# Performance work log

Hardware: AMD Instinct MI355X
Metric: run time of the kernel (lower is better)

## Reference

```python
import jax, jax.numpy as jnp
import numpy as np

B, S, D, NH, NKV, HD = 1, 2048, 4096, 32, 8, 128
SCALE = HD ** -0.5


def setup_inputs() -> dict:
    key = jax.random.key(0)
    ks = jax.random.split(key, 5)
    sd = D ** -0.5
    x = jax.random.normal(ks[0], (B, S, D), jnp.float32)
    Wq = jax.random.normal(ks[1], (D, NH * HD), jnp.float32) * sd
    Wk = jax.random.normal(ks[2], (D, NKV * HD), jnp.float32) * sd
    Wv = jax.random.normal(ks[3], (D, NKV * HD), jnp.float32) * sd
    Wo = jax.random.normal(ks[4], (NH * HD, D), jnp.float32) * sd
    # real rotary tables (rotate-half convention), shape [S, HD]
    inv_freq = 1.0 / (10000.0 ** (np.arange(0, HD, 2, dtype=np.float64) / HD))
    ang = np.outer(np.arange(S, dtype=np.float64), inv_freq)  # [S, HD//2]
    emb = np.concatenate([ang, ang], axis=-1)  # [S, HD]
    cos = jnp.asarray(np.cos(emb), jnp.float32)
    sin = jnp.asarray(np.sin(emb), jnp.float32)
    return dict(x=x, Wq=Wq, Wk=Wk, Wv=Wv, Wo=Wo, cos=cos, sin=sin)


def _rope(t, cos, sin):
    # t: [B,S,H,HD]; cos/sin: [S,HD]
    c = cos[None, :, None, :]
    s = sin[None, :, None, :]
    t1, t2 = jnp.split(t, 2, axis=-1)
    rot = jnp.concatenate([-t2, t1], axis=-1)
    return t * c + rot * s


def _to_i8(t):
    # per-vector absmax quantization over last dim
    scale = 127.0 / jnp.clip(jnp.max(jnp.abs(t), axis=-1, keepdims=True), 1e-5, None)
    q = jnp.clip(jnp.round(t * scale), -128.0, 127.0).astype(jnp.int8)
    return q, scale


def reference(x, Wq, Wk, Wv, Wo, cos, sin):
    q = (x @ Wq).reshape(B, S, NH, HD)
    k = (x @ Wk).reshape(B, S, NKV, HD)
    v = (x @ Wv).reshape(B, S, NKV, HD)
    q = _rope(q, cos, sin)
    k = _rope(k, cos, sin)
    q_i8, q_s = _to_i8(q)          # [B,S,NH,HD], [B,S,NH,1]
    k_i8, k_s = _to_i8(k)          # [B,S,NKV,HD], [B,S,NKV,1]
    rep = NH // NKV                # GQA expansion
    k_i8 = jnp.repeat(k_i8, rep, axis=2)
    k_s = jnp.repeat(k_s, rep, axis=2)
    v = jnp.repeat(v, rep, axis=2)
    # int8 QK^T accumulated in int32 (exact), then per-vector dequant
    scores = jnp.einsum('bshd,bthd->bhst', q_i8, k_i8,
                        preferred_element_type=jnp.int32).astype(jnp.float32)
    q_st = jnp.transpose(q_s, (0, 2, 1, 3))            # [B,NH,S,1]
    k_st = jnp.transpose(k_s, (0, 2, 3, 1))            # [B,NH,1,S]
    scores = scores * (SCALE / (q_st * k_st))
    # causal mask (seq > 1, no cache so total == S)
    mask = jnp.triu(jnp.full((S, S), -jnp.inf, jnp.float32), k=1)
    scores = scores + mask
    attn = jax.nn.softmax(scores, axis=-1)             # [B,NH,S,S]
    out = jnp.einsum('bhst,bthd->bshd', attn, v).reshape(B, S, NH * HD)
    return out @ Wo
```

## Files before the change

### kernel.cpp

```cpp
#include <hip/hip_runtime.h>
#include <hip/hip_bf16.h>

#define S_LEN 2048
#define DMODEL 4096
#define NH 32
#define NKV 8
#define HD 128
#define NQKV 6144
#define VOFF (DMODEL + NKV * HD)
#define ATT_SCALE_L2E 0.1275175213528852f

typedef __bf16 bf16x8 __attribute__((ext_vector_type(8)));
typedef __bf16 bf16x4 __attribute__((ext_vector_type(4)));
typedef float f32x4 __attribute__((ext_vector_type(4)));
typedef int i32x4 __attribute__((ext_vector_type(4)));

template <bool B> struct BoolC { static constexpr bool value = B; };

__device__ __forceinline__ unsigned short f2b(float f) {
  union { float f; unsigned u; } a; a.f = f;
  unsigned u = a.u;
  return (unsigned short)((u + 0x7FFFu + ((u >> 16) & 1u)) >> 16);
}
__device__ __forceinline__ float b2f(unsigned short u) {
  union { unsigned u; float f; } a; a.u = (unsigned)u << 16; return a.f;
}

__device__ __forceinline__ void gl16(const void* g, void* l) {
  __builtin_amdgcn_global_load_lds(
      (const __attribute__((address_space(1))) unsigned int*)g,
      (__attribute__((address_space(3))) unsigned int*)l, 16, 0, 0);
}

__global__ __launch_bounds__(256) void k_prep(const float* __restrict__ x,
                                              const float* __restrict__ Wq,
                                              const float* __restrict__ Wk,
                                              const float* __restrict__ Wv,
                                              const float* __restrict__ Wo,
                                              unsigned short* __restrict__ xb,
                                              unsigned short* __restrict__ wqkv_t,
                                              unsigned short* __restrict__ wo_t) {
  __shared__ float tile[64][65];
  const int id = blockIdx.x;
  if (id >= 10240) {
    int i = (id - 10240) * 256 + threadIdx.x;
    float4 v = ((const float4*)x)[i];
    ushort4 o;
    o.x = f2b(v.x); o.y = f2b(v.y); o.z = f2b(v.z); o.w = f2b(v.w);
    ((ushort4*)xb)[i] = o;
    return;
  }
  const float* W;
  unsigned short* Wt;
  int N, bx, by;
  if (id < 4096)      { W = Wq; Wt = wqkv_t;                         N = 4096; bx = id & 63;          by = id >> 6; }
  else if (id < 5120) { W = Wk; Wt = wqkv_t + (size_t)4096 * 4096;   N = 1024; bx = (id - 4096) & 63; by = (id - 4096) >> 6; }
  else if (id < 6144) { W = Wv; Wt = wqkv_t + (size_t)5120 * 4096;   N = 1024; bx = (id - 5120) & 63; by = (id - 5120) >> 6; }
  else                { W = Wo; Wt = wo_t;                           N = 4096; bx = (id - 6144) & 63; by = (id - 6144) >> 6; }
  const int k0 = bx * 64, n0 = by * 64;
  const int tx = threadIdx.x & 31, ty = threadIdx.x >> 5;
#pragma unroll
  for (int i = 0; i < 8; ++i) {
    int k = ty + i * 8;
    const float* src = W + (size_t)(k0 + k) * N + n0;
    tile[k][tx] = src[tx];
    tile[k][tx + 32] = src[tx + 32];
  }
  __syncthreads();
  int kq = threadIdx.x & 15, nb = threadIdx.x >> 4;
#pragma unroll
  for (int i = 0; i < 4; ++i) {
    int n = nb + i * 16;
    ushort4 o;
    o.x = f2b(tile[kq * 4 + 0][n]);
    o.y = f2b(tile[kq * 4 + 1][n]);
    o.z = f2b(tile[kq * 4 + 2][n]);
    o.w = f2b(tile[kq * 4 + 3][n]);
    *(ushort4*)&Wt[(size_t)(n0 + n) * 4096 + k0 + kq * 4] = o;
  }
}

__global__ __launch_bounds__(256) void k_post(const unsigned short* __restrict__ qkv,
                                              const float* __restrict__ cost,
                                              const float* __restrict__ sint,
                                              signed char* __restrict__ q_i8,
                                              float* __restrict__ q_ds_t,
                                              signed char* __restrict__ k_i8,
                                              float* __restrict__ k_ds_t,
                                              unsigned short* __restrict__ v_t) {
  __shared__ unsigned short tile[64][65];
  const int id = blockIdx.x;
  if (id < 20480) {
    int y = id >> 11, s = id & 2047;
    int wv = threadIdx.x >> 6, l = threadIdx.x & 63;
    int hh = y * 4 + wv;
    const unsigned short* row = qkv + (size_t)s * NQKV;
    int off = (hh < NH) ? hh * HD : DMODEL + (hh - NH) * HD;
    float t1 = b2f(row[off + l]), t2 = b2f(row[off + 64 + l]);
    float c1 = cost[s * HD + l],      sn1 = sint[s * HD + l];
    float c2 = cost[s * HD + 64 + l], sn2 = sint[s * HD + 64 + l];
    float o1 = t1 * c1 - t2 * sn1;
    float o2 = t2 * c2 + t1 * sn2;
    float amax = fmaxf(fabsf(o1), fabsf(o2));
#pragma unroll
    for (int m = 1; m < 64; m <<= 1) amax = fmaxf(amax, __shfl_xor(amax, m));
    amax = fmaxf(amax, 1e-5f);
    float scale = 127.0f / amax;
    float dscale = amax * (1.0f / 127.0f);
    float v1 = fminf(fmaxf(rintf(o1 * scale), -128.f), 127.f);
    float v2 = fminf(fmaxf(rintf(o2 * scale), -128.f), 127.f);
    if (hh < NH) {
      signed char* dst = q_i8 + ((size_t)s * NH + hh) * HD;
      dst[l] = (signed char)v1; dst[l + 64] = (signed char)v2;
      if (l == 0) q_ds_t[(size_t)hh * S_LEN + s] = dscale;
    } else {
      int kh = hh - NH;
      signed char* dst = k_i8 + ((size_t)s * NKV + kh) * HD;
      dst[l] = (signed char)v1; dst[l + 64] = (signed char)v2;
      if (l == 0) k_ds_t[(size_t)kh * S_LEN + s] = dscale;
    }
    return;
  }
  int vid = id - 20480;
  int s0 = (vid & 31) * 64, d0 = ((vid >> 5) & 1) * 64, kvh = vid >> 6;
  int tx = threadIdx.x & 63, ty = threadIdx.x >> 6;
#pragma unroll
  for (int i = 0; i < 16; ++i) {
    int s = ty + i * 4;
    tile[s][tx] = qkv[(size_t)(s0 + s) * NQKV + VOFF + kvh * HD + d0 + tx];
  }
  __syncthreads();
#pragma unroll
  for (int i = 0; i < 16; ++i) {
    int d = ty + i * 4;
    v_t[((size_t)kvh * HD + d0 + d) * S_LEN + s0 + tx] = tile[tx][d];
  }
}

__global__ __launch_bounds__(512, 4) void k_g128x3(const unsigned short* __restrict__ A,
                                                   const unsigned short* __restrict__ B,
                                                   unsigned short* __restrict__ C,
                                                   int M, int N, int K) {
  constexpr int FN = 3;
  extern __shared__ __align__(16) unsigned short smem[];
  char* Sc = (char*)smem;
  const int tid = threadIdx.x;
  const int wvid = tid >> 6, l = tid & 63;
  const int wm = wvid >> 2, wn = wvid & 3;
  const int l15 = l & 15, l4 = l >> 4;

  const int cpx = gridDim.x >> 3;
  const int swz = (blockIdx.x & 7) * cpx + (blockIdx.x >> 3);
  const int mtiles = M >> 7;
  const int m0 = (swz % mtiles) * 128;
  const int n0 = (swz / mtiles) * (FN * 64);

  const int NT = K >> 6;

  const int rsw = (l15 & 7) << 4;
  const int a_base = (wm * 64 + l15) * 128;
  const int b_base = (wn * FN * 16 + l15) * 128;
  const int c0 = (l4 * 16) ^ rsw;
  const int c1 = (64 + l4 * 16) ^ rsw;

  const int srow = l >> 3;
  const int st_k8 = (l & 7) ^ (srow & 7);

  auto stA = [&](int tt) {
    if (tt >= NT) return;
    const unsigned short* g = A + (size_t)(m0 + wvid * 8 + srow) * K + tt * 64 + st_k8 * 8;
    char* lb = Sc + (tt & 1) * 16384 + wvid * 1024;
#pragma unroll
    for (int j = 0; j < 2; ++j)
      gl16(g + (size_t)(j * 64) * K, (unsigned short*)(lb + j * 8192));
  };
  auto stB = [&](int tt) {
    if (tt >= NT) return;
    const unsigned short* g = B + (size_t)(n0 + wvid * 8 + srow) * K + tt * 64 + st_k8 * 8;
    char* lb = Sc + 32768 + (tt & 1) * (FN * 8192) + wvid * 1024;
#pragma unroll
    for (int j = 0; j < FN; ++j)
      gl16(g + (size_t)(j * 64) * K, (unsigned short*)(lb + j * 8192));
  };

  f32x4 acc[4][FN] = {};

  stA(0); stB(0); stA(1);
  if (NT > 1) asm volatile("s_waitcnt vmcnt(2)" ::: "memory");
  else        asm volatile("s_waitcnt vmcnt(0)" ::: "memory");
  __builtin_amdgcn_s_barrier();

  for (int t = 0; t < NT; ++t) {
    const char* Ab = Sc + (t & 1) * 16384;
    const char* Bb = Sc + 32768 + (t & 1) * (FN * 8192);
    stB(t + 1);
    bf16x8 a[4], b[FN];
#pragma unroll
    for (int fm = 0; fm < 4; ++fm) a[fm] = *(const bf16x8*)(Ab + a_base + fm * 2048 + c0);
#pragma unroll
    for (int fn = 0; fn < FN; ++fn) b[fn] = *(const bf16x8*)(Bb + b_base + fn * 2048 + c0);
    __builtin_amdgcn_s_setprio(1);
#pragma unroll
    for (int fm = 0; fm < 4; ++fm)
#pragma unroll
      for (int fn = 0; fn < FN; ++fn)
        acc[fm][fn] = __builtin_amdgcn_mfma_f32_16x16x32_bf16(a[fm], b[fn], acc[fm][fn], 0, 0, 0);
    __builtin_amdgcn_s_setprio(0);
#pragma unroll
    for (int fm = 0; fm < 4; ++fm) a[fm] = *(const bf16x8*)(Ab + a_base + fm * 2048 + c1);
#pragma unroll
    for (int fn = 0; fn < FN; ++fn) b[fn] = *(const bf16x8*)(Bb + b_base + fn * 2048 + c1);
    __builtin_amdgcn_s_setprio(1);
#pragma unroll
    for (int fm = 0; fm < 4; ++fm)
#pragma unroll
      for (int fn = 0; fn < FN; ++fn)
        acc[fm][fn] = __builtin_amdgcn_mfma_f32_16x16x32_bf16(a[fm], b[fn], acc[fm][fn], 0, 0, 0);
    __builtin_amdgcn_s_setprio(0);
    __builtin_amdgcn_s_barrier();
    stA(t + 2);
    if (t + 1 < NT) {
      if (t + 1 == NT - 1) asm volatile("s_waitcnt vmcnt(0)" ::: "memory");
      else                 asm volatile("s_waitcnt vmcnt(2)" ::: "memory");
      __builtin_amdgcn_s_barrier();
    }
  }

#pragma unroll
  for (int fm = 0; fm < 4; ++fm) {
    int row0 = m0 + wm * 64 + fm * 16 + l4 * 4;
#pragma unroll
    for (int fn = 0; fn < FN; ++fn) {
      int col = n0 + wn * FN * 16 + fn * 16 + l15;
#pragma unroll
      for (int r = 0; r < 4; ++r)
        C[(size_t)(row0 + r) * N + col] = f2b(acc[fm][fn][r]);
    }
  }
}

__global__ __launch_bounds__(512, 4) void k_gksplit(const unsigned short* __restrict__ A,
                                                    const unsigned short* __restrict__ B,
                                                    float* __restrict__ C,
                                                    int M, int N, int K) {
  extern __shared__ __align__(16) unsigned short smem[];
  char* Sc = (char*)smem;
  const int tid = threadIdx.x;
  const int wvid = tid >> 6, l = tid & 63;
  const int wm = wvid & 1, wn = (wvid >> 1) & 1, wk = wvid >> 2;
  const int l15 = l & 15, l4 = l >> 4;

  const int cpx = gridDim.x >> 3;
  const int swz = (blockIdx.x & 7) * cpx + (blockIdx.x >> 3);
  const int mtiles = M >> 7;
  const int m0 = (swz % mtiles) * 128;
  const int n0 = (swz / mtiles) * 128;

  const int NT = K >> 6;

  const int rsw = (l15 & 7) << 4;
  const int a_base = (wm * 64 + l15) * 128;
  const int b_base = (wn * 64 + l15) * 128;
  const int ck = (wk * 64 + l4 * 16) ^ rsw;

  const int srow = l >> 3;
  const int st_k8 = (l & 7) ^ (srow & 7);

  auto stA = [&](int tt) {
    if (tt >= NT) return;
    const unsigned short* g = A + (size_t)(m0 + wvid * 8 + srow) * K + tt * 64 + st_k8 * 8;
    char* lb = Sc + (tt & 1) * 16384 + wvid * 1024;
#pragma unroll
    for (int j = 0; j < 2; ++j)
      gl16(g + (size_t)(j * 64) * K, (unsigned short*)(lb + j * 8192));
  };
  auto stB = [&](int tt) {
    if (tt >= NT) return;
    const unsigned short* g = B + (size_t)(n0 + wvid * 8 + srow) * K + tt * 64 + st_k8 * 8;
    char* lb = Sc + 32768 + (tt & 1) * 16384 + wvid * 1024;
#pragma unroll
    for (int j = 0; j < 2; ++j)
      gl16(g + (size_t)(j * 64) * K, (unsigned short*)(lb + j * 8192));
  };

  f32x4 acc[4][4] = {};

  stA(0); stB(0); stA(1);
  if (NT > 1) asm volatile("s_waitcnt vmcnt(2)" ::: "memory");
  else        asm volatile("s_waitcnt vmcnt(0)" ::: "memory");
  __builtin_amdgcn_s_barrier();

  for (int t = 0; t < NT; ++t) {
    const char* Ab = Sc + (t & 1) * 16384;
    const char* Bb = Sc + 32768 + (t & 1) * 16384;
    stB(t + 1);
    bf16x8 a[4], b[4];
#pragma unroll
    for (int fm = 0; fm < 4; ++fm) a[fm] = *(const bf16x8*)(Ab + a_base + fm * 2048 + ck);
#pragma unroll
    for (int fn = 0; fn < 4; ++fn) b[fn] = *(const bf16x8*)(Bb + b_base + fn * 2048 + ck);
    __builtin_amdgcn_s_setprio(1);
#pragma unroll
    for (int fm = 0; fm < 4; ++fm)
#pragma unroll
      for (int fn = 0; fn < 4; ++fn)
        acc[fm][fn] = __builtin_amdgcn_mfma_f32_16x16x32_bf16(a[fm], b[fn], acc[fm][fn], 0, 0, 0);
    __builtin_amdgcn_s_setprio(0);
    __builtin_amdgcn_s_barrier();
    stA(t + 2);
    if (t + 1 < NT) {
      if (t + 1 == NT - 1) asm volatile("s_waitcnt vmcnt(0)" ::: "memory");
      else                 asm volatile("s_waitcnt vmcnt(2)" ::: "memory");
      __builtin_amdgcn_s_barrier();
    }
  }

  char* xch = Sc + (wm * 2 + wn) * 16384;
  if (wk == 1) {
#pragma unroll
    for (int fm = 0; fm < 4; ++fm)
#pragma unroll
      for (int fn = 0; fn < 4; ++fn)
        *(f32x4*)(xch + (fm * 4 + fn) * 1024 + l * 16) = acc[fm][fn];
  }
  __syncthreads();
  if (wk == 0) {
#pragma unroll
    for (int fm = 0; fm < 4; ++fm) {
      int row0 = m0 + wm * 64 + fm * 16 + l4 * 4;
#pragma unroll
      for (int fn = 0; fn < 4; ++fn) {
        f32x4 o = *(const f32x4*)(xch + (fm * 4 + fn) * 1024 + l * 16);
        int col = n0 + wn * 64 + fn * 16 + l15;
#pragma unroll
        for (int r = 0; r < 4; ++r)
          C[(size_t)(row0 + r) * N + col] = acc[fm][fn][r] + o[r];
      }
    }
  }
}

__global__ __launch_bounds__(512, 4) void k_attn(const signed char* __restrict__ q_i8,
                                                 const float* __restrict__ q_ds_t,
                                                 const signed char* __restrict__ k_i8,
                                                 const float* __restrict__ k_ds_t,
                                                 const unsigned short* __restrict__ v_t,
                                                 unsigned short* __restrict__ o_bf) {
  __shared__ __align__(16) signed char K_lds[2][8192];
  __shared__ __align__(16) unsigned short V_lds[2][8192];
  __shared__ __align__(16) unsigned short P_lds[8][1024];

  const int bid = blockIdx.x;
  const int kvh = bid & 7;
  const int qt = 63 - (bid >> 3);
  const int tid = threadIdx.x, wv = tid >> 6, l = tid & 63;
  const int l15 = l & 15, l4 = l >> 4;
  const int h = kvh * 4 + (wv & 3);
  const int rh = wv >> 2;

  auto stage = [&](int b, int kt) {
    {
      int key = tid >> 3, g = tid & 7;
      int colb = (g * 16) ^ ((key & 7) << 4);
      const signed char* src = k_i8 + ((size_t)(kt * 64 + key) * NKV + kvh) * HD + colb;
      gl16(src, &K_lds[b][tid * 16]);
    }
    const unsigned short* vB = v_t + (size_t)kvh * HD * S_LEN + (size_t)kt * 64;
#pragma unroll
    for (int j = 0; j < 2; ++j) {
      int wi = j * 8 + wv;
      int slot = wi * 64 + l;
      int d = slot >> 3;
      int ckb = ((slot & 7) * 16) ^ ((d & 7) << 4);
      gl16(vB + (size_t)d * S_LEN + (ckb >> 1), &V_lds[b][wi * 512]);
    }
  };

  const int qrow_lo = qt * 32 + rh * 16;
  const int qg = qrow_lo + l15;
  const int crow = qrow_lo + l4 * 4;

  i32x4 qf[2];
  {
    const signed char* qp = q_i8 + ((size_t)qg * NH + h) * HD + l4 * 16;
    qf[0] = *(const i32x4*)(qp);
    qf[1] = *(const i32x4*)(qp + 64);
  }
  const float qsS = ATT_SCALE_L2E * q_ds_t[(size_t)h * S_LEN + qg];

  float m_run = -3.0e38f, l_run = 0.f;
  f32x4 o_acc[8] = {};

  const int nkt = (qt >> 1) + 1;
  stage(0, 0);
  __syncthreads();

  const int psw = (l15 & 7) << 4;

  auto tileBody = [&](auto mc, int kt) {
    constexpr bool MASKED = decltype(mc)::value;
    const int cur = kt & 1;
    f32x4 ksd[4];
    {
      const f32x4* kdp = (const f32x4*)(k_ds_t + (size_t)kvh * S_LEN + kt * 64 + l4 * 4);
#pragma unroll
      for (int nt = 0; nt < 4; ++nt) ksd[nt] = kdp[nt * 4];
    }
    if (kt + 1 < nkt) stage(cur ^ 1, kt + 1);

    i32x4 sacc[4] = {};
#pragma unroll
    for (int nt = 0; nt < 4; ++nt) {
      int key = nt * 16 + l15;
#pragma unroll
      for (int kd = 0; kd < 2; ++kd) {
        int byte = key * 128 + kd * 64 + l4 * 16;
        byte ^= (key & 7) << 4;
        i32x4 kf = *(const i32x4*)(&K_lds[cur][0] + byte);
        sacc[nt] = __builtin_amdgcn_mfma_i32_16x16x64_i8(kf, qf[kd], sacc[nt], 0, 0, 0);
      }
    }

    float p[4][4];
    float tmax = -3.0e38f;
#pragma unroll
    for (int nt = 0; nt < 4; ++nt) {
#pragma unroll
      for (int r = 0; r < 4; ++r) {
        float sc = (float)sacc[nt][r] * (qsS * ksd[nt][r]);
        if constexpr (MASKED) {
          int keyg = kt * 64 + nt * 16 + l4 * 4 + r;
          sc = (keyg <= qg) ? sc : -3.0e38f;
        }
        p[nt][r] = sc;
        tmax = fmaxf(tmax, sc);
      }
    }
    tmax = fmaxf(tmax, __shfl_xor(tmax, 16));
    tmax = fmaxf(tmax, __shfl_xor(tmax, 32));

    float nm = fmaxf(m_run, tmax);
    bool need = tmax > m_run + 11.0f;
    if (__ballot(need)) {
      float corr = __builtin_amdgcn_exp2f(m_run - nm);
      m_run = nm;
      l_run *= corr;
      float cq[4];
#pragma unroll
      for (int r = 0; r < 4; ++r) cq[r] = __shfl(corr, (l & 48) | (l4 * 4 + r));
#pragma unroll
      for (int dt = 0; dt < 8; ++dt)
#pragma unroll
        for (int r = 0; r < 4; ++r) o_acc[dt][r] *= cq[r];
    }

    float psum = 0.f;
#pragma unroll
    for (int nt = 0; nt < 4; ++nt)
#pragma unroll
      for (int r = 0; r < 4; ++r) {
        float e = __builtin_amdgcn_exp2f(p[nt][r] - m_run);
        p[nt][r] = e;
        psum += e;
      }
    psum += __shfl_xor(psum, 16);
    psum += __shfl_xor(psum, 32);
    l_run += psum;

#pragma unroll
    for (int nt = 0; nt < 4; ++nt) {
      bf16x4 pk;
      pk[0] = (__bf16)p[nt][0]; pk[1] = (__bf16)p[nt][1];
      pk[2] = (__bf16)p[nt][2]; pk[3] = (__bf16)p[nt][3];
      int bw = l15 * 128 + ((nt * 32 + l4 * 8) ^ psw);
      *(bf16x4*)((char*)&P_lds[wv][0] + bw) = pk;
    }
    bf16x8 pa[2];
#pragma unroll
    for (int kc = 0; kc < 2; ++kc) {
      int br = l15 * 128 + ((kc * 64 + l4 * 16) ^ psw);
      pa[kc] = *(const bf16x8*)((const char*)&P_lds[wv][0] + br);
    }

#pragma unroll
    for (int dt = 0; dt < 8; ++dt) {
      int d = dt * 16 + l15;
      int swzv = (d & 7) << 4;
#pragma unroll
      for (int kc = 0; kc < 2; ++kc) {
        int byte = d * 128 + ((kc * 64 + l4 * 16) ^ swzv);
        bf16x8 vb = *(const bf16x8*)((const char*)&V_lds[cur][0] + byte);
        o_acc[dt] = __builtin_amdgcn_mfma_f32_16x16x32_bf16(pa[kc], vb, o_acc[dt], 0, 0, 0);
      }
    }
    __syncthreads();
  };

  for (int kt = 0; kt + 1 < nkt; ++kt) tileBody(BoolC<false>{}, kt);
  tileBody(BoolC<true>{}, nkt - 1);

  float inv = 1.0f / l_run;
  float invq[4];
#pragma unroll
  for (int r = 0; r < 4; ++r) invq[r] = __shfl(inv, (l & 48) | (l4 * 4 + r));
#pragma unroll
  for (int dt = 0; dt < 8; ++dt)
#pragma unroll
    for (int r = 0; r < 4; ++r)
      o_bf[(size_t)(crow + r) * (NH * HD) + h * HD + dt * 16 + l15] =
          f2b(o_acc[dt][r] * invq[r]);
}

extern "C" void kernel_launch(void* const* d_in, const int* in_sizes, int n_in,
                              void* d_out, int out_size, void* d_ws, size_t ws_size,
                              hipStream_t stream) {
  const float* x    = (const float*)d_in[0];
  const float* Wq   = (const float*)d_in[1];
  const float* Wk   = (const float*)d_in[2];
  const float* Wv   = (const float*)d_in[3];
  const float* Wo   = (const float*)d_in[4];
  const float* cost = (const float*)d_in[5];
  const float* sint = (const float*)d_in[6];
  float* out = (float*)d_out;
  char* ws = (char*)d_ws;

  unsigned short* xb     = (unsigned short*)(ws);
  unsigned short* wqkv_t = (unsigned short*)(ws + 16777216);
  unsigned short* wo_t   = (unsigned short*)(ws + 67108864);
  unsigned short* qkv    = (unsigned short*)(ws + 100663296);
  signed char*    q_i8   = (signed char*)(ws + 150994944);
  signed char*    k_i8   = (signed char*)(ws + 167772160);
  float*          q_ds_t = (float*)(ws + 176160768);
  float*          k_ds_t = (float*)(ws + 176422912);
  unsigned short* o_bf   = (unsigned short*)(ws + 176488448);
  unsigned short* v_t    = (unsigned short*)(ws);

  hipFuncSetAttribute((const void*)k_g128x3,
                      hipFuncAttributeMaxDynamicSharedMemorySize, 81920);
  hipFuncSetAttribute((const void*)k_gksplit,
                      hipFuncAttributeMaxDynamicSharedMemorySize, 65536);

  k_prep<<<dim3(18432), 256, 0, stream>>>(x, Wq, Wk, Wv, Wo, xb, wqkv_t, wo_t);
  k_g128x3<<<dim3(512), 512, 81920, stream>>>(xb, wqkv_t, qkv, 2048, 6144, 4096);
  k_post<<<dim3(20992), 256, 0, stream>>>(qkv, cost, sint, q_i8, q_ds_t, k_i8, k_ds_t, v_t);
  k_attn<<<dim3(512), 512, 0, stream>>>(q_i8, q_ds_t, k_i8, k_ds_t, v_t, o_bf);
  k_gksplit<<<dim3(512), 512, 65536, stream>>>(o_bf, wo_t, out, 2048, 4096, 4096);
}
```

Before: 288.5 us.

## Enlarge QKV GEMM tile to 256x192 with quadrant-ordered MFMA schedule

Replaces the 128x192 QKV projection GEMM with a 256x192 tile per block, halving the grid to 256 blocks. Each wave now computes a 2x2 set of 32x48 sub-tiles, and the loop interleaves LDS fragment loads and global prefetches with four MFMA phases separated by barriers. The aim is more arithmetic per byte loaded and better overlap of loads with compute. In exchange it uses 112 KB of LDS and more accumulator registers, dropping occupancy to 2 blocks per CU, and 256 blocks may underfill the CUs on this device.

```diff
diff --git a/kernel.cpp b/kernel.cpp
--- a/kernel.cpp
+++ b/kernel.cpp
@@ -137,106 +137,155 @@
   }
 }
 
-__global__ __launch_bounds__(512, 4) void k_g128x3(const unsigned short* __restrict__ A,
-                                                   const unsigned short* __restrict__ B,
-                                                   unsigned short* __restrict__ C,
-                                                   int M, int N, int K) {
-  constexpr int FN = 3;
+__global__ __launch_bounds__(512, 2) void k_g256x192(const unsigned short* __restrict__ A,
+                                                     const unsigned short* __restrict__ B,
+                                                     unsigned short* __restrict__ C,
+                                                     int M, int N, int K) {
   extern __shared__ __align__(16) unsigned short smem[];
   char* Sc = (char*)smem;
   const int tid = threadIdx.x;
   const int wvid = tid >> 6, l = tid & 63;
-  const int wm = wvid >> 2, wn = wvid & 3;
+  const int wm = wvid >> 1, wn = wvid & 1;
   const int l15 = l & 15, l4 = l >> 4;
 
   const int cpx = gridDim.x >> 3;
   const int swz = (blockIdx.x & 7) * cpx + (blockIdx.x >> 3);
-  const int mtiles = M >> 7;
-  const int m0 = (swz % mtiles) * 128;
-  const int n0 = (swz / mtiles) * (FN * 64);
+  const int mtiles = M >> 8;
+  const int m0 = (swz % mtiles) * 256;
+  const int n0 = (swz / mtiles) * 192;
 
   const int NT = K >> 6;
 
   const int rsw = (l15 & 7) << 4;
-  const int a_base = (wm * 64 + l15) * 128;
-  const int b_base = (wn * FN * 16 + l15) * 128;
+  const int a_base = (wm * 32 + l15) * 128;
+  const int b_base = (wn * 48 + l15) * 128;
   const int c0 = (l4 * 16) ^ rsw;
   const int c1 = (64 + l4 * 16) ^ rsw;
 
   const int srow = l >> 3;
   const int st_k8 = (l & 7) ^ (srow & 7);
 
-  auto stA = [&](int tt) {
+  auto stA = [&](int tt, int h) {
     if (tt >= NT) return;
-    const unsigned short* g = A + (size_t)(m0 + wvid * 8 + srow) * K + tt * 64 + st_k8 * 8;
-    char* lb = Sc + (tt & 1) * 16384 + wvid * 1024;
+    const unsigned short* g = A + (size_t)(m0 + h * 128 + wvid * 8 + srow) * K + tt * 64 + st_k8 * 8;
+    char* lb = Sc + (tt & 1) * 32768 + h * 16384 + wvid * 1024;
 #pragma unroll
     for (int j = 0; j < 2; ++j)
-      gl16(g + (size_t)(j * 64) * K, (unsigned short*)(lb + j * 8192));
+      gl16(g + (size_t)(j * 64) * K, lb + j * 8192);
   };
   auto stB = [&](int tt) {
     if (tt >= NT) return;
     const unsigned short* g = B + (size_t)(n0 + wvid * 8 + srow) * K + tt * 64 + st_k8 * 8;
-    char* lb = Sc + 32768 + (tt & 1) * (FN * 8192) + wvid * 1024;
-#pragma unroll
-    for (int j = 0; j < FN; ++j)
-      gl16(g + (size_t)(j * 64) * K, (unsigned short*)(lb + j * 8192));
+    char* lb = Sc + 65536 + (tt & 1) * 24576 + wvid * 1024;
+#pragma unroll
+    for (int j = 0; j < 3; ++j)
+      gl16(g + (size_t)(j * 64) * K, lb + j * 8192);
   };
 
-  f32x4 acc[4][FN] = {};
-
-  stA(0); stB(0); stA(1);
-  if (NT > 1) asm volatile("s_waitcnt vmcnt(2)" ::: "memory");
+  f32x4 acc[2][2][2][3] = {};
+
+  stA(0, 0); stA(0, 1); stB(0);
+  stA(1, 0); stA(1, 1);
+  if (NT > 1) asm volatile("s_waitcnt vmcnt(4)" ::: "memory");
   else        asm volatile("s_waitcnt vmcnt(0)" ::: "memory");
   __builtin_amdgcn_s_barrier();
 
   for (int t = 0; t < NT; ++t) {
-    const char* Ab = Sc + (t & 1) * 16384;
-    const char* Bb = Sc + 32768 + (t & 1) * (FN * 8192);
+    const char* Ab = Sc + (t & 1) * 32768;
+    const char* Bb = Sc + 65536 + (t & 1) * 24576;
+    bf16x8 a[2][2], b0[3][2], b1[3][2];
+
+#pragma unroll
+    for (int fm = 0; fm < 2; ++fm) {
+      a[fm][0] = *(const bf16x8*)(Ab + a_base + fm * 2048 + c0);
+      a[fm][1] = *(const bf16x8*)(Ab + a_base + fm * 2048 + c1);
+    }
+#pragma unroll
+    for (int fn = 0; fn < 3; ++fn) {
+      b0[fn][0] = *(const bf16x8*)(Bb + b_base + fn * 2048 + c0);
+      b0[fn][1] = *(const bf16x8*)(Bb + b_base + fn * 2048 + c1);
+    }
     stB(t + 1);
-    bf16x8 a[4], b[FN];
-#pragma unroll
-    for (int fm = 0; fm < 4; ++fm) a[fm] = *(const bf16x8*)(Ab + a_base + fm * 2048 + c0);
-#pragma unroll
-    for (int fn = 0; fn < FN; ++fn) b[fn] = *(const bf16x8*)(Bb + b_base + fn * 2048 + c0);
+    __builtin_amdgcn_s_barrier();
     __builtin_amdgcn_s_setprio(1);
 #pragma unroll
-    for (int fm = 0; fm < 4; ++fm)
-#pragma unroll
-      for (int fn = 0; fn < FN; ++fn)
-        acc[fm][fn] = __builtin_amdgcn_mfma_f32_16x16x32_bf16(a[fm], b[fn], acc[fm][fn], 0, 0, 0);
+    for (int fm = 0; fm < 2; ++fm)
+#pragma unroll
+      for (int fn = 0; fn < 3; ++fn)
+#pragma unroll
+        for (int ks = 0; ks < 2; ++ks)
+          acc[0][fm][0][fn] = __builtin_amdgcn_mfma_f32_16x16x32_bf16(a[fm][ks], b0[fn][ks], acc[0][fm][0][fn], 0, 0, 0);
     __builtin_amdgcn_s_setprio(0);
-#pragma unroll
-    for (int fm = 0; fm < 4; ++fm) a[fm] = *(const bf16x8*)(Ab + a_base + fm * 2048 + c1);
-#pragma unroll
-    for (int fn = 0; fn < FN; ++fn) b[fn] = *(const bf16x8*)(Bb + b_base + fn * 2048 + c1);
+    __builtin_amdgcn_s_barrier();
+
+#pragma unroll
+    for (int fn = 0; fn < 3; ++fn) {
+      b1[fn][0] = *(const bf16x8*)(Bb + 12288 + b_base + fn * 2048 + c0);
+      b1[fn][1] = *(const bf16x8*)(Bb + 12288 + b_base + fn * 2048 + c1);
+    }
+    stA(t + 2, 0);
+    __builtin_amdgcn_s_barrier();
     __builtin_amdgcn_s_setprio(1);
 #pragma unroll
-    for (int fm = 0; fm < 4; ++fm)
-#pragma unroll
-      for (int fn = 0; fn < FN; ++fn)
-        acc[fm][fn] = __builtin_amdgcn_mfma_f32_16x16x32_bf16(a[fm], b[fn], acc[fm][fn], 0, 0, 0);
+    for (int fm = 0; fm < 2; ++fm)
+#pragma unroll
+      for (int fn = 0; fn < 3; ++fn)
+#pragma unroll
+        for (int ks = 0; ks < 2; ++ks)
+          acc[0][fm][1][fn] = __builtin_amdgcn_mfma_f32_16x16x32_bf16(a[fm][ks], b1[fn][ks], acc[0][fm][1][fn], 0, 0, 0);
     __builtin_amdgcn_s_setprio(0);
     __builtin_amdgcn_s_barrier();
-    stA(t + 2);
+
+#pragma unroll
+    for (int fm = 0; fm < 2; ++fm) {
+      a[fm][0] = *(const bf16x8*)(Ab + 16384 + a_base + fm * 2048 + c0);
+      a[fm][1] = *(const bf16x8*)(Ab + 16384 + a_base + fm * 2048 + c1);
+    }
+    __builtin_amdgcn_s_barrier();
+    __builtin_amdgcn_s_setprio(1);
+#pragma unroll
+    for (int fm = 0; fm < 2; ++fm)
+#pragma unroll
+      for (int fn = 0; fn < 3; ++fn)
+#pragma unroll
+        for (int ks = 0; ks < 2; ++ks)
+          acc[1][fm][1][fn] = __builtin_amdgcn_mfma_f32_16x16x32_bf16(a[fm][ks], b1[fn][ks], acc[1][fm][1][fn], 0, 0, 0);
+    __builtin_amdgcn_s_setprio(0);
+    __builtin_amdgcn_s_barrier();
+
+    stA(t + 2, 1);
+    __builtin_amdgcn_s_barrier();
+    __builtin_amdgcn_s_setprio(1);
+#pragma unroll
+    for (int fm = 0; fm < 2; ++fm)
+#pragma unroll
+      for (int fn = 0; fn < 3; ++fn)
+#pragma unroll
+        for (int ks = 0; ks < 2; ++ks)
+          acc[1][fm][0][fn] = __builtin_amdgcn_mfma_f32_16x16x32_bf16(a[fm][ks], b0[fn][ks], acc[1][fm][0][fn], 0, 0, 0);
+    __builtin_amdgcn_s_setprio(0);
     if (t + 1 < NT) {
       if (t + 1 == NT - 1) asm volatile("s_waitcnt vmcnt(0)" ::: "memory");
-      else                 asm volatile("s_waitcnt vmcnt(2)" ::: "memory");
-      __builtin_amdgcn_s_barrier();
-    }
-  }
-
-#pragma unroll
-  for (int fm = 0; fm < 4; ++fm) {
-    int row0 = m0 + wm * 64 + fm * 16 + l4 * 4;
-#pragma unroll
-    for (int fn = 0; fn < FN; ++fn) {
-      int col = n0 + wn * FN * 16 + fn * 16 + l15;
-#pragma unroll
-      for (int r = 0; r < 4; ++r)
-        C[(size_t)(row0 + r) * N + col] = f2b(acc[fm][fn][r]);
-    }
-  }
+      else                 asm volatile("s_waitcnt vmcnt(4)" ::: "memory");
+    }
+    __builtin_amdgcn_s_barrier();
+  }
+
+#pragma unroll
+  for (int ah = 0; ah < 2; ++ah)
+#pragma unroll
+    for (int fm = 0; fm < 2; ++fm) {
+      int row0 = m0 + ah * 128 + wm * 32 + fm * 16 + l4 * 4;
+#pragma unroll
+      for (int bh = 0; bh < 2; ++bh)
+#pragma unroll
+        for (int fn = 0; fn < 3; ++fn) {
+          int col = n0 + bh * 96 + wn * 48 + fn * 16 + l15;
+#pragma unroll
+          for (int r = 0; r < 4; ++r)
+            C[(size_t)(row0 + r) * N + col] = f2b(acc[ah][fm][bh][fn][r]);
+        }
+    }
 }
 
 __global__ __launch_bounds__(512, 4) void k_gksplit(const unsigned short* __restrict__ A,
@@ -272,7 +321,7 @@
     char* lb = Sc + (tt & 1) * 16384 + wvid * 1024;
 #pragma unroll
     for (int j = 0; j < 2; ++j)
-      gl16(g + (size_t)(j * 64) * K, (unsigned short*)(lb + j * 8192));
+      gl16(g + (size_t)(j * 64) * K, lb + j * 8192);
   };
   auto stB = [&](int tt) {
     if (tt >= NT) return;
@@ -280,7 +329,7 @@
     char* lb = Sc + 32768 + (tt & 1) * 16384 + wvid * 1024;
 #pragma unroll
     for (int j = 0; j < 2; ++j)
-      gl16(g + (size_t)(j * 64) * K, (unsigned short*)(lb + j * 8192));
+      gl16(g + (size_t)(j * 64) * K, lb + j * 8192);
   };
 
   f32x4 acc[4][4] = {};
@@ -535,13 +584,13 @@
   unsigned short* o_bf   = (unsigned short*)(ws + 176488448);
   unsigned short* v_t    = (unsigned short*)(ws);
 
-  hipFuncSetAttribute((const void*)k_g128x3,
-                      hipFuncAttributeMaxDynamicSharedMemorySize, 81920);
+  hipFuncSetAttribute((const void*)k_g256x192,
+                      hipFuncAttributeMaxDynamicSharedMemorySize, 114688);
   hipFuncSetAttribute((const void*)k_gksplit,
                       hipFuncAttributeMaxDynamicSharedMemorySize, 65536);
 
   k_prep<<<dim3(18432), 256, 0, stream>>>(x, Wq, Wk, Wv, Wo, xb, wqkv_t, wo_t);
-  k_g128x3<<<dim3(512), 512, 81920, stream>>>(xb, wqkv_t, qkv, 2048, 6144, 4096);
+  k_g256x192<<<dim3(256), 512, 114688, stream>>>(xb, wqkv_t, qkv, 2048, 6144, 4096);
   k_post<<<dim3(20992), 256, 0, stream>>>(qkv, cost, sint, q_i8, q_ds_t, k_i8, k_ds_t, v_t);
   k_attn<<<dim3(512), 512, 0, stream>>>(q_i8, q_ds_t, k_i8, k_ds_t, v_t, o_bf);
   k_gksplit<<<dim3(512), 512, 65536, stream>>>(o_bf, wo_t, out, 2048, 4096, 4096);
```

Measured after the change: 286.5 us. About the same (-0.7%).
